# Performance work log

Measured on AMD Instinct MI355X. Metric: run time of the kernel, lower is better.

The kernel has to match this reference:

```python
import jax, jax.numpy as jnp
import numpy as np

N_E = 1024
E_DIM = 256
BETA = 0.25
DECAY = 0.99
EPS = 1e-5


def setup_inputs() -> dict:
    key = jax.random.key(0)
    k1, k2 = jax.random.split(key)
    z = jax.random.normal(k1, (16, E_DIM, 64, 64), dtype=jnp.float32)
    # embedding.weight.data.uniform_(-1/n_e, 1/n_e)
    weight = jax.random.uniform(k2, (N_E, E_DIM), dtype=jnp.float32,
                                minval=-1.0 / N_E, maxval=1.0 / N_E)
    cluster_size = jnp.zeros((N_E,), dtype=jnp.float32)
    embedding_avg = weight  # clone of initial weight
    return {"z": z, "weight": weight, "cluster_size": cluster_size,
            "embedding_avg": embedding_avg}


def reference(z, weight, cluster_size, embedding_avg):
    B, C, H, W = z.shape  # C == e_dim
    zp = jnp.transpose(z, (0, 2, 3, 1))          # [B,H,W,C]
    zf = zp.reshape(-1, C)                       # [N, C], N = B*H*W

    # ||z||^2 + ||e||^2 - 2 z e^T  -> [N, n_e]
    d = (jnp.sum(zf * zf, axis=1, keepdims=True)
         + jnp.sum(weight * weight, axis=1)
         - 2.0 * jnp.matmul(zf, weight.T))
    idx = jnp.argmin(d, axis=1)                  # [N] int

    z_q = weight[idx].reshape(zp.shape)          # [B,H,W,C]

    # EMA codebook update (training branch), computed with scatter-sums
    n_e = weight.shape[0]
    counts = jax.ops.segment_sum(jnp.ones(zf.shape[0], dtype=zf.dtype),
                                 idx, num_segments=n_e)        # encodings.sum(0)
    new_cluster_size = cluster_size * DECAY + (1.0 - DECAY) * counts
    n = jnp.sum(new_cluster_size)
    cs_smoothed = (new_cluster_size + EPS) / (n + n_e * EPS) * n
    dw = jax.ops.segment_sum(zf, idx, num_segments=n_e)        # encodings.T @ zf
    new_embedding_avg = embedding_avg * DECAY + (1.0 - DECAY) * dw
    new_weight = new_embedding_avg / cs_smoothed[:, None]

    loss = BETA * jnp.mean((jax.lax.stop_gradient(z_q) - zp) ** 2)
    z_q_st = zp + jax.lax.stop_gradient(z_q - zp)   # straight-through
    out = jnp.transpose(z_q_st, (0, 3, 1, 2))        # back to NCHW
    return out, loss, idx, new_cluster_size, new_embedding_avg, new_weight
```

## Files before the change

kernel.cpp:

```cpp
#include <hip/hip_runtime.h>
#include <hip/hip_bf16.h>

typedef unsigned short ushort_t;
typedef __attribute__((ext_vector_type(8))) _Float16 half8;
typedef __attribute__((ext_vector_type(4))) float f32x4;

#define NB    16
#define NC    256
#define NHW   4096
#define NPIX  65536
#define NE    1024
#define BETA  0.25f
#define DECAY 0.99f
#define EPS_  1e-5f
#define GAP_FLAG 1.25e-4f

#define OFF_LOSS 16777216
#define OFF_IDXF 16777217
#define OFF_NCS  16842753
#define OFF_NEA  16843777
#define OFF_NW   17105921

#define WS_WSUM  0
#define WS_CSSM  1024
#define WS_LPART 2048
#define WS_CNT   3072
#define WS_FLAGS 3104
#define WS_LIST  5152
#define WS_WF16  40960
#define WS_ZF16  (WS_WF16 + 131072)
#define WS_IDXI  (WS_ZF16 + 8388608)
#define WS_END   (WS_IDXI + 65536)

__device__ __forceinline__ float sq_nofma(float x) {
    float s = x * x;
    asm volatile("" : "+v"(s));
    return s;
}

__device__ __forceinline__ float np_pair128_sq(const float* __restrict__ a) {
    float r[8];
    #pragma unroll
    for (int m = 0; m < 8; ++m) r[m] = sq_nofma(a[m]);
    for (int i = 8; i < 128; i += 8) {
        #pragma unroll
        for (int m = 0; m < 8; ++m) r[m] += sq_nofma(a[i + m]);
    }
    return ((r[0] + r[1]) + (r[2] + r[3])) + ((r[4] + r[5]) + (r[6] + r[7]));
}

__device__ __forceinline__ void gload16(const void* g, void* ldsp) {
    __builtin_amdgcn_global_load_lds((const __attribute__((address_space(1))) unsigned int*)g,
                                     (__attribute__((address_space(3))) unsigned int*)ldsp,
                                     16, 0, 0);
}

__global__ __launch_bounds__(256) void init_kernel(float* __restrict__ ncs,
                                                   int* __restrict__ cnt) {
    int gid = blockIdx.x * 256 + threadIdx.x;
    if (gid < NE) ncs[gid] = 0.0f;
    if (gid == 0) cnt[0] = 0;
}

__global__ __launch_bounds__(64) void wsum_kernel(const float* __restrict__ w,
                                                  float* __restrict__ wsum) {
    int j = blockIdx.x * 64 + threadIdx.x;
    const float* wr = w + (size_t)j * NC;
    wsum[j] = np_pair128_sq(wr) + np_pair128_sq(wr + 128);
}

__global__ __launch_bounds__(256) void wpack_kernel(const float* __restrict__ w,
                                                    _Float16* __restrict__ wf) {
    int i = blockIdx.x * 256 + threadIdx.x;
    wf[i] = (_Float16)(w[i] * 1024.0f);
}

__global__ __launch_bounds__(256) void zpack_kernel(const float* __restrict__ z,
                                                    _Float16* __restrict__ zf) {
    __shared__ float zs[64 * 65];
    const int t = threadIdx.x;
    const int P0 = blockIdx.x * 64;
    const int b = P0 >> 12, hw0 = P0 & (NHW - 1);
    const int K0 = blockIdx.y * 64;
    const int hw = t & 63, cq = t >> 6;
    const float* zb = z + (size_t)b * (NC * NHW) + hw0 + hw;
    #pragma unroll
    for (int i = 0; i < 16; ++i) {
        int kl = cq * 16 + i;
        zs[hw * 65 + kl] = zb[(size_t)(K0 + kl) * NHW];
    }
    __syncthreads();
    const int p = t >> 2, kq = t & 3;
    size_t obase = (size_t)(P0 + p) * NC + K0 + kq * 16;
    #pragma unroll
    for (int h2 = 0; h2 < 2; ++h2) {
        half8 v;
        #pragma unroll
        for (int j2 = 0; j2 < 8; ++j2)
            v[j2] = (_Float16)zs[p * 65 + kq * 16 + h2 * 8 + j2];
        *(half8*)&zf[obase + h2 * 8] = v;
    }
}

__global__ __launch_bounds__(256) void gemm2_kernel(const _Float16* __restrict__ wf,
                                                    const _Float16* __restrict__ zf,
                                                    const float* __restrict__ wsum,
                                                    float* __restrict__ idxf,
                                                    int* __restrict__ idxi,
                                                    ushort_t* __restrict__ list,
                                                    int* __restrict__ cnt) {
    __shared__ __align__(16) _Float16 zt[128 * 256];
    __shared__ __align__(16) _Float16 wt[128 * 32];
    __shared__ float bvx[256], svx[256];
    __shared__ int   bix[256];
    __shared__ float rbv[128], rsv[128];
    __shared__ int   rbi[128];

    const int t = threadIdx.x;
    const int l = t & 63;
    const int w = t >> 6;
    const int P0 = blockIdx.x * 128;
    const int wc = w >> 1, wp = w & 1;

    #pragma unroll
    for (int i = 0; i < 16; ++i) {
        int row = w * 32 + i * 2 + (l >> 5);
        int gc = (l & 31) ^ (row & 7);
        gload16(zf + (size_t)(P0 + row) * NC + gc * 8,
                &zt[w * 8192 + i * 512 + l * 8]);
    }
    if (t < 128) { rbv[t] = 3.4e38f; rsv[t] = 3.4e38f; rbi[t] = 0; }
    __syncthreads();

    for (int ct = 0; ct < 8; ++ct) {
        f32x4 acc[4][4];
        #pragma unroll
        for (int m = 0; m < 4; ++m)
            #pragma unroll
            for (int n = 0; n < 4; ++n)
                #pragma unroll
                for (int e = 0; e < 4; ++e) acc[m][n][e] = 0.0f;

        for (int ks = 0; ks < 8; ++ks) {
            if (ks) __syncthreads();
            #pragma unroll
            for (int i = 0; i < 2; ++i) {
                int row = w * 32 + i * 16 + (l >> 2);
                int gc = (l & 3) ^ ((l >> 3) & 3);
                gload16(wf + (size_t)(ct * 128 + row) * NC + ks * 32 + gc * 8,
                        &wt[w * 1024 + i * 512 + l * 8]);
            }
            __syncthreads();

            half8 a[4], b[4];
            #pragma unroll
            for (int m = 0; m < 4; ++m) {
                int row = wc * 64 + m * 16 + (l & 15);
                int g = (l >> 4) ^ ((row >> 1) & 3);
                a[m] = *(const half8*)&wt[row * 32 + g * 8];
            }
            #pragma unroll
            for (int n = 0; n < 4; ++n) {
                int row = wp * 64 + n * 16 + (l & 15);
                int chunk = (ks * 4 + (l >> 4)) ^ (row & 7);
                b[n] = *(const half8*)&zt[row * 256 + chunk * 8];
            }
            #pragma unroll
            for (int m = 0; m < 4; ++m)
                #pragma unroll
                for (int n = 0; n < 4; ++n)
                    acc[m][n] = __builtin_amdgcn_mfma_f32_16x16x32_f16(a[m], b[n], acc[m][n], 0, 0, 0);
        }

        float en[4][4];
        #pragma unroll
        for (int m = 0; m < 4; ++m)
            #pragma unroll
            for (int r = 0; r < 4; ++r)
                en[m][r] = wsum[ct * 128 + wc * 64 + m * 16 + (l >> 4) * 4 + r];

        #pragma unroll
        for (int n = 0; n < 4; ++n) {
            float bv = 3.4e38f, sv = 3.4e38f;
            int bi = 0;
            #pragma unroll
            for (int m = 0; m < 4; ++m)
                #pragma unroll
                for (int r = 0; r < 4; ++r) {
                    float s = en[m][r] - acc[m][n][r] * 0.001953125f;
                    int code = ct * 128 + wc * 64 + m * 16 + (l >> 4) * 4 + r;
                    if (s < bv) { sv = bv; bv = s; bi = code; }
                    else if (s < sv) sv = s;
                }
            #pragma unroll
            for (int x = 16; x <= 32; x <<= 1) {
                float v2 = __shfl_xor(bv, x);
                float s2 = __shfl_xor(sv, x);
                int   i2 = __shfl_xor(bi, x);
                if (v2 < bv || (v2 == bv && i2 < bi)) { sv = fminf(bv, s2); bv = v2; bi = i2; }
                else sv = fminf(sv, v2);
            }
            if ((l >> 4) == 0) {
                int lp = wp * 64 + n * 16 + l;
                bvx[wc * 128 + lp] = bv;
                svx[wc * 128 + lp] = sv;
                bix[wc * 128 + lp] = bi;
            }
        }
        __syncthreads();
        if (t < 128) {
            float bv = bvx[t], sv = svx[t];
            int bi = bix[t];
            float v2 = bvx[128 + t], s2 = svx[128 + t];
            int i2 = bix[128 + t];
            if (v2 < bv || (v2 == bv && i2 < bi)) { sv = fminf(bv, s2); bv = v2; bi = i2; }
            else sv = fminf(sv, v2);
            if (bv < rbv[t]) { rsv[t] = fminf(rbv[t], sv); rbv[t] = bv; rbi[t] = bi; }
            else rsv[t] = fminf(rsv[t], bv);
        }
        __syncthreads();
    }

    if (t < 128) {
        int pix = P0 + t;
        idxf[pix] = (float)rbi[t];
        idxi[pix] = rbi[t];
        if (rsv[t] - rbv[t] < GAP_FLAG) {
            int pos = atomicAdd(cnt, 1);
            list[pos] = (ushort_t)pix;
        }
    }
}

__global__ __launch_bounds__(256) void argmin_kernel(const float* __restrict__ z,
                                                     const float* __restrict__ w,
                                                     const float* __restrict__ enorm,
                                                     float* __restrict__ idxf,
                                                     int* __restrict__ idxi,
                                                     unsigned long long* __restrict__ flags) {
    __shared__ __align__(16) float smem[64 * 68 + 128 * 68];
    float* zt = smem;
    float* wt = smem + 64 * 68;
    const int t = threadIdx.x;
    const int pr = t & 7;
    const int cr = t >> 3;
    const int P0 = blockIdx.x * 64;
    const int b = P0 >> 12;
    const int hw0 = P0 & (NHW - 1);
    const float* zb = z + (size_t)b * (NC * NHW) + hw0;
    float bestv[8], secv[8];
    int besti[8];
    #pragma unroll
    for (int i = 0; i < 8; ++i) { bestv[i] = 3.4e38f; secv[i] = 3.4e38f; besti[i] = 0; }
    for (int cc = 0; cc < 8; ++cc) {
        float acc[8][4];
        #pragma unroll
        for (int i = 0; i < 8; ++i)
            #pragma unroll
            for (int j = 0; j < 4; ++j) acc[i][j] = 0.0f;
        for (int kc = 0; kc < 4; ++kc) {
            {
                int p = t & 63;
                int k0 = (t >> 6) * 16;
                int f2 = ((p >> 3) & 3) << 2;
                #pragma unroll
                for (int i = 0; i < 16; ++i) {
                    int k = k0 + i;
                    zt[p * 68 + (k ^ f2)] = zb[(size_t)(kc * 64 + k) * NHW + p];
                }
            }
            {
                #pragma unroll
                for (int i = 0; i < 8; ++i) {
                    int f = t + 256 * i;
                    int jj = f >> 4;
                    int k4 = f & 15;
                    float4 v = *(const float4*)&w[(size_t)(cc * 128 + jj) * NC + kc * 64 + k4 * 4];
                    *(float4*)&wt[jj * 68 + k4 * 4] = v;
                }
            }
            __syncthreads();
            #pragma unroll 2
            for (int k = 0; k < 64; k += 4) {
                float4 za[8], wb[4];
                #pragma unroll
                for (int i = 0; i < 8; ++i)
                    za[i] = *(float4*)&zt[(pr + 8 * i) * 68 + (k ^ ((i & 3) << 2))];
                #pragma unroll
                for (int j = 0; j < 4; ++j)
                    wb[j] = *(float4*)&wt[(cr + 32 * j) * 68 + k];
                #pragma unroll
                for (int i = 0; i < 8; ++i)
                    #pragma unroll
                    for (int j = 0; j < 4; ++j)
                        acc[i][j] += za[i].x * wb[j].x + za[i].y * wb[j].y +
                                     za[i].z * wb[j].z + za[i].w * wb[j].w;
            }
            __syncthreads();
        }
        #pragma unroll
        for (int j = 0; j < 4; ++j) {
            int code = cc * 128 + cr + 32 * j;
            float enj = enorm[code];
            #pragma unroll
            for (int i = 0; i < 8; ++i) {
                float s = enj - 2.0f * acc[i][j];
                if (s < bestv[i]) { secv[i] = bestv[i]; bestv[i] = s; besti[i] = code; }
                else if (s < secv[i]) secv[i] = s;
            }
        }
    }
    float* rv = smem;
    int* ri = (int*)(smem + 2048);
    float* rs = smem + 4096;
    #pragma unroll
    for (int i = 0; i < 8; ++i) {
        int p = pr + 8 * i;
        rv[p * 32 + cr] = bestv[i];
        ri[p * 32 + cr] = besti[i];
        rs[p * 32 + cr] = secv[i];
    }
    __syncthreads();
    if (t < 64) {
        int p = t;
        float bv = rv[p * 32], sv = rs[p * 32];
        int bi = ri[p * 32];
        for (int s2 = 1; s2 < 32; ++s2) {
            float v = rv[p * 32 + s2];
            float v2 = rs[p * 32 + s2];
            int ii = ri[p * 32 + s2];
            if (v < bv) { sv = bv; bv = v; bi = ii; }
            else {
                if (v < sv) sv = v;
                if (v == bv && ii < bi) bi = ii;
            }
            if (v2 < sv) sv = v2;
        }
        idxf[P0 + p] = (float)bi;
        idxi[P0 + p] = bi;
        unsigned long long mask = __ballot((sv - bv) < GAP_FLAG);
        if (t == 0) flags[blockIdx.x] = mask;
    }
}

__global__ __launch_bounds__(256) void gather_kernel(const unsigned long long* __restrict__ flags,
                                                     ushort_t* __restrict__ list,
                                                     int* __restrict__ cnt) {
    int p = blockIdx.x * 256 + threadIdx.x;
    unsigned long long m = flags[p >> 6];
    if ((m >> (p & 63)) & 1ULL) {
        int pos = atomicAdd(cnt, 1);
        list[pos] = (ushort_t)p;
    }
}

__global__ __launch_bounds__(256) void fixup3_kernel(const float* __restrict__ z,
                                                     const float* __restrict__ w,
                                                     const float* __restrict__ wsum,
                                                     const ushort_t* __restrict__ list,
                                                     const int* __restrict__ cnt,
                                                     float* __restrict__ idxf,
                                                     int* __restrict__ idxi) {
    const int count = cnt[0];
    if (count == 0) return;
    const int ngroups = (count + 7) >> 3;
    const int t = threadIdx.x;

    __shared__ __align__(16) char smem_raw[16384 + 8192];
    double (*zd)[NC] = (double(*)[NC])smem_raw;
    float  (*zf)[NC] = (float(*)[NC])(smem_raw + 16384);
    float* rbv = (float*)(smem_raw + 16384);
    int*   rbi = (int*)smem_raw;
    __shared__ float zs_sh[8];
    __shared__ int   pix_sh[8];
    __shared__ float r2v[8][32];
    __shared__ int   r2i[8][32];

    for (int g = blockIdx.x; g < ngroups; g += gridDim.x) {
        if (t < 8) {
            int i = g * 8 + t;
            pix_sh[t] = (i < count) ? (int)list[i] : (int)list[0];
        }
        __syncthreads();
        #pragma unroll
        for (int px = 0; px < 8; ++px) {
            int p = pix_sh[px];
            int b = p >> 12, hw = p & (NHW - 1);
            float zv = z[(size_t)b * (NC * NHW) + (size_t)t * NHW + hw];
            zf[px][t] = zv;
            zd[px][t] = (double)zv;
        }
        __syncthreads();
        if (t < 8) zs_sh[t] = np_pair128_sq(zf[t]) + np_pair128_sq(zf[t] + 128);
        __syncthreads();

        float zs_reg[8];
        #pragma unroll
        for (int px = 0; px < 8; ++px) zs_reg[px] = zs_sh[px];

        float bvr[8];
        int   bir[8];
        #pragma unroll
        for (int px = 0; px < 8; ++px) { bvr[px] = 3.4e38f; bir[px] = 0; }

        #pragma unroll
        for (int jo = 0; jo < 2; ++jo) {
            const int j0 = t + jo * 512;
            const int j1 = j0 + 256;
            const float* wr0 = w + (size_t)j0 * NC;
            const float* wr1 = w + (size_t)j1 * NC;
            double acc0[8], acc1[8];
            #pragma unroll
            for (int px = 0; px < 8; ++px) { acc0[px] = 0.0; acc1[px] = 0.0; }
            for (int k = 0; k < NC; k += 4) {
                float4 wa = *(const float4*)&wr0[k];
                float4 wb = *(const float4*)&wr1[k];
                const float* wap = (const float*)&wa;
                const float* wbp = (const float*)&wb;
                #pragma unroll
                for (int e = 0; e < 4; ++e) {
                    double wea = (double)wap[e];
                    double web = (double)wbp[e];
                    #pragma unroll
                    for (int px = 0; px < 8; ++px) {
                        double zv = zd[px][k + e];
                        acc0[px] += wea * zv;
                        acc1[px] += web * zv;
                    }
                }
            }
            float ws0 = wsum[j0], ws1 = wsum[j1];
            #pragma unroll
            for (int px = 0; px < 8; ++px) {
                float m0 = (float)acc0[px];
                float s10 = zs_reg[px] + ws0;
                float d0 = s10 - 2.0f * m0;
                if (d0 < bvr[px] || (d0 == bvr[px] && j0 < bir[px])) { bvr[px] = d0; bir[px] = j0; }
                float m1 = (float)acc1[px];
                float s11 = zs_reg[px] + ws1;
                float d1 = s11 - 2.0f * m1;
                if (d1 < bvr[px] || (d1 == bvr[px] && j1 < bir[px])) { bvr[px] = d1; bir[px] = j1; }
            }
        }
        __syncthreads();
        #pragma unroll
        for (int px = 0; px < 8; ++px) {
            rbv[px * 256 + t] = bvr[px];
            rbi[px * 256 + t] = bir[px];
        }
        __syncthreads();
        {
            int px = t >> 5, s = t & 31;
            float bv = rbv[px * 256 + s * 8];
            int   bi = rbi[px * 256 + s * 8];
            #pragma unroll
            for (int e = 1; e < 8; ++e) {
                float v2 = rbv[px * 256 + s * 8 + e];
                int   i2 = rbi[px * 256 + s * 8 + e];
                if (v2 < bv || (v2 == bv && i2 < bi)) { bv = v2; bi = i2; }
            }
            r2v[px][s] = bv;
            r2i[px][s] = bi;
        }
        __syncthreads();
        if (t < 8) {
            float bv = r2v[t][0];
            int   bi = r2i[t][0];
            for (int s = 1; s < 32; ++s) {
                float v2 = r2v[t][s];
                int   i2 = r2i[t][s];
                if (v2 < bv || (v2 == bv && i2 < bi)) { bv = v2; bi = i2; }
            }
            if (g * 8 + t < count) {
                idxf[pix_sh[t]] = (float)bi;
                idxi[pix_sh[t]] = bi;
            }
        }
        __syncthreads();
    }
}

__global__ __launch_bounds__(1024) void hist_kernel(const int* __restrict__ idxi,
                                                    float* __restrict__ ncs) {
    __shared__ int h[NE];
    int t = threadIdx.x;
    h[t] = 0;
    __syncthreads();
    int gid = blockIdx.x * 1024 + t;
    #pragma unroll
    for (int i = 0; i < 4; ++i) atomicAdd(&h[idxi[gid + i * 16384]], 1);
    __syncthreads();
    if (h[t]) atomicAdd(&ncs[t], (float)h[t]);
}

__global__ __launch_bounds__(1024) void outdw_kernel(const float* __restrict__ z,
                                                     const float* __restrict__ w,
                                                     const int* __restrict__ idxi,
                                                     float* __restrict__ outq,
                                                     float* __restrict__ dw0,
                                                     float* __restrict__ dw1,
                                                     float* __restrict__ lpart) {
    __shared__ float acc[NE];
    __shared__ float wcol[NE];
    __shared__ float ls[16];
    const int c = blockIdx.x;
    const int part = blockIdx.y;
    const int t = threadIdx.x;
    acc[t] = 0.0f;
    wcol[t] = w[(size_t)t * NC + c];
    __syncthreads();
    const float* zc = z + (size_t)c * NHW;
    float* oc = outq + (size_t)c * NHW;
    float lsum = 0.0f;
    #pragma unroll
    for (int i = 0; i < 8; ++i) {
        int b = part * 8 + i;
        int p0 = b * 4096 + t * 4;
        size_t a = (size_t)b * (NC * NHW) + t * 4;
        float4 zv = *(const float4*)&zc[a];
        int4 iv = *(const int4*)&idxi[p0];
        float4 ov;
        ov.x = wcol[iv.x]; ov.y = wcol[iv.y]; ov.z = wcol[iv.z]; ov.w = wcol[iv.w];
        *(float4*)&oc[a] = ov;
        float d0 = ov.x - zv.x, d1 = ov.y - zv.y, d2 = ov.z - zv.z, d3 = ov.w - zv.w;
        lsum += d0 * d0 + d1 * d1 + d2 * d2 + d3 * d3;
        atomicAdd(&acc[iv.x], zv.x);
        atomicAdd(&acc[iv.y], zv.y);
        atomicAdd(&acc[iv.z], zv.z);
        atomicAdd(&acc[iv.w], zv.w);
    }
    #pragma unroll
    for (int off = 32; off > 0; off >>= 1) lsum += __shfl_down(lsum, off);
    if ((t & 63) == 0) ls[t >> 6] = lsum;
    __syncthreads();
    if (t == 0) {
        float s = 0.0f;
        #pragma unroll
        for (int q = 0; q < 16; ++q) s += ls[q];
        lpart[c * 2 + part] = s;
    }
    float* dwp = part ? dw1 : dw0;
    dwp[(size_t)t * NC + c] = acc[t];
}

__global__ __launch_bounds__(1024) void finalize_kernel(const float* __restrict__ cs,
                                                        const float* __restrict__ lpart,
                                                        float* __restrict__ ncs,
                                                        float* __restrict__ cssm,
                                                        float* __restrict__ loss) {
    int t = threadIdx.x;
    float cnt = ncs[t];
    float v = cs[t] * DECAY + (1.0f - DECAY) * cnt;
    ncs[t] = v;
    __shared__ float red[1024];
    red[t] = v;
    __syncthreads();
    for (int s = 512; s > 0; s >>= 1) {
        if (t < s) red[t] += red[t + s];
        __syncthreads();
    }
    float n = red[0];
    __syncthreads();
    cssm[t] = (v + EPS_) / (n + (float)NE * EPS_) * n;
    red[t] = (t < 512) ? lpart[t] : 0.0f;
    __syncthreads();
    for (int s = 512; s > 0; s >>= 1) {
        if (t < s) red[t] += red[t + s];
        __syncthreads();
    }
    if (t == 0) loss[0] = BETA * red[0] / 16777216.0f;
}

__global__ __launch_bounds__(256) void neaw_kernel(const float* __restrict__ ea,
                                                   const float* __restrict__ cssm,
                                                   float* __restrict__ nea,
                                                   float* __restrict__ nw) {
    int lin = blockIdx.x * 256 + threadIdx.x;
    float dw = nea[lin] + nw[lin];
    float v = DECAY * ea[lin] + (1.0f - DECAY) * dw;
    nea[lin] = v;
    nw[lin] = v / cssm[lin >> 8];
}

extern "C" void kernel_launch(void* const* d_in, const int* in_sizes, int n_in,
                              void* d_out, int out_size, void* d_ws, size_t ws_size,
                              hipStream_t stream) {
    const float* z  = (const float*)d_in[0];
    const float* w  = (const float*)d_in[1];
    const float* cs = (const float*)d_in[2];
    const float* ea = (const float*)d_in[3];

    float* out  = (float*)d_out;
    float* loss = out + OFF_LOSS;
    float* idxf = out + OFF_IDXF;
    float* ncs  = out + OFF_NCS;
    float* nea  = out + OFF_NEA;
    float* nw   = out + OFF_NW;

    float* wsf = (float*)d_ws;
    float* wsum = wsf + WS_WSUM;
    float* cssm = wsf + WS_CSSM;
    float* lpart = wsf + WS_LPART;
    int* cnt = (int*)(wsf + WS_CNT);
    unsigned long long* flags = (unsigned long long*)(wsf + WS_FLAGS);
    ushort_t* list = (ushort_t*)(wsf + WS_LIST);
    int* idxi = (int*)(wsf + WS_IDXI);

    hipLaunchKernelGGL(init_kernel, dim3(4), dim3(256), 0, stream, ncs, cnt);
    hipLaunchKernelGGL(wsum_kernel, dim3(16), dim3(64), 0, stream, w, wsum);

    if (ws_size >= (size_t)WS_END * 4) {
        _Float16* wf16 = (_Float16*)(wsf + WS_WF16);
        _Float16* zf16 = (_Float16*)(wsf + WS_ZF16);
        hipLaunchKernelGGL(wpack_kernel, dim3(1024), dim3(256), 0, stream, w, wf16);
        hipLaunchKernelGGL(zpack_kernel, dim3(1024, 4), dim3(256), 0, stream, z, zf16);
        hipLaunchKernelGGL(gemm2_kernel, dim3(512), dim3(256), 0, stream,
                           wf16, zf16, wsum, idxf, idxi, list, cnt);
    } else {
        hipLaunchKernelGGL(argmin_kernel, dim3(1024), dim3(256), 0, stream, z, w, wsum, idxf, idxi, flags);
        hipLaunchKernelGGL(gather_kernel, dim3(256), dim3(256), 0, stream, flags, list, cnt);
    }

    hipLaunchKernelGGL(fixup3_kernel, dim3(256), dim3(256), 0, stream, z, w, wsum, list, cnt, idxf, idxi);
    hipLaunchKernelGGL(hist_kernel, dim3(16), dim3(1024), 0, stream, idxi, ncs);
    hipLaunchKernelGGL(outdw_kernel, dim3(256, 2), dim3(1024), 0, stream, z, w, idxi, out, nea, nw, lpart);
    hipLaunchKernelGGL(finalize_kernel, dim3(1), dim3(1024), 0, stream, cs, lpart, ncs, cssm, loss);
    hipLaunchKernelGGL(neaw_kernel, dim3(1024), dim3(256), 0, stream, ea, cssm, nea, nw);
}
```

Measured before the change: 299.0 us.

## Fuse histogram into GEMM epilogue and fold init into wsum kernel

Removes the separate init and histogram kernels. The argmin GEMM epilogue now builds a per-block LDS histogram and atomically adds it into the cluster-size counts, and the fixup kernel corrects counts with paired -1/+1 atomics when it changes an index. The outdw kernel also batches four float4 loads before use and gets a min-blocks launch bound. This saves two launches and one pass over the index array, at the cost of extra global atomics and ordering dependencies between the fused kernels.

```diff
diff --git a/kernel.cpp b/kernel.cpp
--- a/kernel.cpp
+++ b/kernel.cpp
@@ -55,18 +55,15 @@
                                      16, 0, 0);
 }
 
-__global__ __launch_bounds__(256) void init_kernel(float* __restrict__ ncs,
-                                                   int* __restrict__ cnt) {
-    int gid = blockIdx.x * 256 + threadIdx.x;
-    if (gid < NE) ncs[gid] = 0.0f;
-    if (gid == 0) cnt[0] = 0;
-}
-
 __global__ __launch_bounds__(64) void wsum_kernel(const float* __restrict__ w,
-                                                  float* __restrict__ wsum) {
+                                                  float* __restrict__ wsum,
+                                                  float* __restrict__ ncs,
+                                                  int* __restrict__ cnt) {
     int j = blockIdx.x * 64 + threadIdx.x;
     const float* wr = w + (size_t)j * NC;
     wsum[j] = np_pair128_sq(wr) + np_pair128_sq(wr + 128);
+    ncs[j] = 0.0f;
+    if (j == 0) cnt[0] = 0;
 }
 
 __global__ __launch_bounds__(256) void wpack_kernel(const float* __restrict__ w,
@@ -108,7 +105,8 @@
                                                     float* __restrict__ idxf,
                                                     int* __restrict__ idxi,
                                                     ushort_t* __restrict__ list,
-                                                    int* __restrict__ cnt) {
+                                                    int* __restrict__ cnt,
+                                                    float* __restrict__ ncs) {
     __shared__ __align__(16) _Float16 zt[128 * 256];
     __shared__ __align__(16) _Float16 wt[128 * 32];
     __shared__ float bvx[256], svx[256];
@@ -221,14 +219,25 @@
         __syncthreads();
     }
 
+    int* h = (int*)zt;
+    #pragma unroll
+    for (int e = 0; e < 4; ++e) h[t + e * 256] = 0;
+    __syncthreads();
     if (t < 128) {
         int pix = P0 + t;
         idxf[pix] = (float)rbi[t];
         idxi[pix] = rbi[t];
+        atomicAdd(&h[rbi[t]], 1);
         if (rsv[t] - rbv[t] < GAP_FLAG) {
             int pos = atomicAdd(cnt, 1);
             list[pos] = (ushort_t)pix;
         }
+    }
+    __syncthreads();
+    #pragma unroll
+    for (int e = 0; e < 4; ++e) {
+        int v = h[t + e * 256];
+        if (v) atomicAdd(&ncs[t + e * 256], (float)v);
     }
 }
 
@@ -354,13 +363,27 @@
     }
 }
 
+__global__ __launch_bounds__(1024) void hist_kernel(const int* __restrict__ idxi,
+                                                    float* __restrict__ ncs) {
+    __shared__ int h[NE];
+    int t = threadIdx.x;
+    h[t] = 0;
+    __syncthreads();
+    int gid = blockIdx.x * 1024 + t;
+    #pragma unroll
+    for (int i = 0; i < 4; ++i) atomicAdd(&h[idxi[gid + i * 16384]], 1);
+    __syncthreads();
+    if (h[t]) atomicAdd(&ncs[t], (float)h[t]);
+}
+
 __global__ __launch_bounds__(256) void fixup3_kernel(const float* __restrict__ z,
                                                      const float* __restrict__ w,
                                                      const float* __restrict__ wsum,
                                                      const ushort_t* __restrict__ list,
                                                      const int* __restrict__ cnt,
                                                      float* __restrict__ idxf,
-                                                     int* __restrict__ idxi) {
+                                                     int* __restrict__ idxi,
+                                                     float* __restrict__ ncs) {
     const int count = cnt[0];
     if (count == 0) return;
     const int ngroups = (count + 7) >> 3;
@@ -472,34 +495,27 @@
                 if (v2 < bv || (v2 == bv && i2 < bi)) { bv = v2; bi = i2; }
             }
             if (g * 8 + t < count) {
-                idxf[pix_sh[t]] = (float)bi;
-                idxi[pix_sh[t]] = bi;
-            }
-        }
-        __syncthreads();
-    }
-}
-
-__global__ __launch_bounds__(1024) void hist_kernel(const int* __restrict__ idxi,
-                                                    float* __restrict__ ncs) {
-    __shared__ int h[NE];
-    int t = threadIdx.x;
-    h[t] = 0;
-    __syncthreads();
-    int gid = blockIdx.x * 1024 + t;
-    #pragma unroll
-    for (int i = 0; i < 4; ++i) atomicAdd(&h[idxi[gid + i * 16384]], 1);
-    __syncthreads();
-    if (h[t]) atomicAdd(&ncs[t], (float)h[t]);
-}
-
-__global__ __launch_bounds__(1024) void outdw_kernel(const float* __restrict__ z,
-                                                     const float* __restrict__ w,
-                                                     const int* __restrict__ idxi,
-                                                     float* __restrict__ outq,
-                                                     float* __restrict__ dw0,
-                                                     float* __restrict__ dw1,
-                                                     float* __restrict__ lpart) {
+                int p = pix_sh[t];
+                int old = idxi[p];
+                if (old != bi) {
+                    idxf[p] = (float)bi;
+                    idxi[p] = bi;
+                    atomicAdd(&ncs[old], -1.0f);
+                    atomicAdd(&ncs[bi], 1.0f);
+                }
+            }
+        }
+        __syncthreads();
+    }
+}
+
+__global__ __launch_bounds__(1024, 8) void outdw_kernel(const float* __restrict__ z,
+                                                        const float* __restrict__ w,
+                                                        const int* __restrict__ idxi,
+                                                        float* __restrict__ outq,
+                                                        float* __restrict__ dw0,
+                                                        float* __restrict__ dw1,
+                                                        float* __restrict__ lpart) {
     __shared__ float acc[NE];
     __shared__ float wcol[NE];
     __shared__ float ls[16];
@@ -513,21 +529,30 @@
     float* oc = outq + (size_t)c * NHW;
     float lsum = 0.0f;
     #pragma unroll
-    for (int i = 0; i < 8; ++i) {
-        int b = part * 8 + i;
-        int p0 = b * 4096 + t * 4;
-        size_t a = (size_t)b * (NC * NHW) + t * 4;
-        float4 zv = *(const float4*)&zc[a];
-        int4 iv = *(const int4*)&idxi[p0];
-        float4 ov;
-        ov.x = wcol[iv.x]; ov.y = wcol[iv.y]; ov.z = wcol[iv.z]; ov.w = wcol[iv.w];
-        *(float4*)&oc[a] = ov;
-        float d0 = ov.x - zv.x, d1 = ov.y - zv.y, d2 = ov.z - zv.z, d3 = ov.w - zv.w;
-        lsum += d0 * d0 + d1 * d1 + d2 * d2 + d3 * d3;
-        atomicAdd(&acc[iv.x], zv.x);
-        atomicAdd(&acc[iv.y], zv.y);
-        atomicAdd(&acc[iv.z], zv.z);
-        atomicAdd(&acc[iv.w], zv.w);
+    for (int half = 0; half < 2; ++half) {
+        float4 zv[4];
+        int4   iv[4];
+        #pragma unroll
+        for (int i = 0; i < 4; ++i) {
+            int b = part * 8 + half * 4 + i;
+            zv[i] = *(const float4*)&zc[(size_t)b * (NC * NHW) + t * 4];
+            iv[i] = *(const int4*)&idxi[b * 4096 + t * 4];
+        }
+        #pragma unroll
+        for (int i = 0; i < 4; ++i) {
+            int b = part * 8 + half * 4 + i;
+            float4 ov;
+            ov.x = wcol[iv[i].x]; ov.y = wcol[iv[i].y];
+            ov.z = wcol[iv[i].z]; ov.w = wcol[iv[i].w];
+            *(float4*)&oc[(size_t)b * (NC * NHW) + t * 4] = ov;
+            float d0 = ov.x - zv[i].x, d1 = ov.y - zv[i].y;
+            float d2 = ov.z - zv[i].z, d3 = ov.w - zv[i].w;
+            lsum += d0 * d0 + d1 * d1 + d2 * d2 + d3 * d3;
+            atomicAdd(&acc[iv[i].x], zv[i].x);
+            atomicAdd(&acc[iv[i].y], zv[i].y);
+            atomicAdd(&acc[iv[i].z], zv[i].z);
+            atomicAdd(&acc[iv[i].w], zv[i].w);
+        }
     }
     #pragma unroll
     for (int off = 32; off > 0; off >>= 1) lsum += __shfl_down(lsum, off);
@@ -606,8 +631,7 @@
     ushort_t* list = (ushort_t*)(wsf + WS_LIST);
     int* idxi = (int*)(wsf + WS_IDXI);
 
-    hipLaunchKernelGGL(init_kernel, dim3(4), dim3(256), 0, stream, ncs, cnt);
-    hipLaunchKernelGGL(wsum_kernel, dim3(16), dim3(64), 0, stream, w, wsum);
+    hipLaunchKernelGGL(wsum_kernel, dim3(16), dim3(64), 0, stream, w, wsum, ncs, cnt);
 
     if (ws_size >= (size_t)WS_END * 4) {
         _Float16* wf16 = (_Float16*)(wsf + WS_WF16);
@@ -615,14 +639,17 @@
         hipLaunchKernelGGL(wpack_kernel, dim3(1024), dim3(256), 0, stream, w, wf16);
         hipLaunchKernelGGL(zpack_kernel, dim3(1024, 4), dim3(256), 0, stream, z, zf16);
         hipLaunchKernelGGL(gemm2_kernel, dim3(512), dim3(256), 0, stream,
-                           wf16, zf16, wsum, idxf, idxi, list, cnt);
+                           wf16, zf16, wsum, idxf, idxi, list, cnt, ncs);
+        hipLaunchKernelGGL(fixup3_kernel, dim3(256), dim3(256), 0, stream,
+                           z, w, wsum, list, cnt, idxf, idxi, ncs);
     } else {
         hipLaunchKernelGGL(argmin_kernel, dim3(1024), dim3(256), 0, stream, z, w, wsum, idxf, idxi, flags);
         hipLaunchKernelGGL(gather_kernel, dim3(256), dim3(256), 0, stream, flags, list, cnt);
-    }
-
-    hipLaunchKernelGGL(fixup3_kernel, dim3(256), dim3(256), 0, stream, z, w, wsum, list, cnt, idxf, idxi);
-    hipLaunchKernelGGL(hist_kernel, dim3(16), dim3(1024), 0, stream, idxi, ncs);
+        hipLaunchKernelGGL(hist_kernel, dim3(16), dim3(1024), 0, stream, idxi, ncs);
+        hipLaunchKernelGGL(fixup3_kernel, dim3(256), dim3(256), 0, stream,
+                           z, w, wsum, list, cnt, idxf, idxi, ncs);
+    }
+
     hipLaunchKernelGGL(outdw_kernel, dim3(256, 2), dim3(1024), 0, stream, z, w, idxi, out, nea, nw, lpart);
     hipLaunchKernelGGL(finalize_kernel, dim3(1), dim3(1024), 0, stream, cs, lpart, ncs, cssm, loss);
     hipLaunchKernelGGL(neaw_kernel, dim3(1024), dim3(256), 0, stream, ea, cssm, nea, nw);
```

Result: no change. 300.5 us (+0.5%).
